# Optimization experiments

Hardware: AMD Instinct MI355X
Metric: run time of the kernel (lower is better)

The kernel has to match this reference:

```python
import jax, jax.numpy as jnp
import numpy as np

ALPHA = 0.02      # LeakyReLU negative slope
N_GRAPHS = 128    # number of graphs in the batch (global_mean_pool segments)
NEG_INF = jnp.float32(-9e15)


def _gat_head(x, mask, W, a1, a2):
    # One GraphAttentionLayer (no dropout: eval mode).
    Wh = x @ W                                   # [N, h]
    f1 = Wh @ a1                                 # [N] = a[:h] . Wh_i
    f2 = Wh @ a2                                 # [N] = a[h:] . Wh_j
    e = jax.nn.leaky_relu(f1[:, None] + f2[None, :], negative_slope=ALPHA)  # [N, N]
    e = jnp.where(mask, e, NEG_INF)              # adjacency-masked logits
    att = jax.nn.softmax(e, axis=-1)             # row-wise over neighbors
    return att @ Wh                              # [N, h]


def reference(x, edge_index, batch, W_heads, a1_heads, a2_heads,
              W_out, a1_out, a2_out, W1, b1, W2, b2):
    N = x.shape[0]
    # adj[src, dst] = 1 via scatter, exactly as the torch code
    adj = jnp.zeros((N, N), dtype=jnp.float32).at[edge_index[0], edge_index[1]].set(1.0)
    mask = adj > 0
    # multi-head GAT, heads vmapped: [H, N, h]
    heads = jax.vmap(_gat_head, in_axes=(None, None, 0, 0, 0))(
        x, mask, W_heads, a1_heads, a2_heads)
    heads = jax.nn.elu(heads)                    # concat=True applies elu per head
    h = jnp.transpose(heads, (1, 0, 2)).reshape(N, -1)   # concat -> [N, H*h]
    out = jax.nn.elu(_gat_head(h, mask, W_out, a1_out, a2_out))  # out_att + outer elu
    # global mean pool over graphs
    seg_sum = jax.ops.segment_sum(out, batch, num_segments=N_GRAPHS)
    counts = jax.ops.segment_sum(jnp.ones((N,), jnp.float32), batch, num_segments=N_GRAPHS)
    pooled = seg_sum / jnp.maximum(counts, 1.0)[:, None]          # [G, att_out]
    # MLP head
    hid = jax.nn.relu(pooled @ W1 + b1)
    return hid @ W2 + b2                                          # [G, nout]


def setup_inputs() -> dict:
    key = jax.random.key(0)
    ks = jax.random.split(key, 12)
    N, F, H, HID, OUT, MLP, NOUT, E = 2048, 300, 20, 600, 1000, 1000, 768, 32768
    s = 0.05
    return {
        "x": jax.random.normal(ks[0], (N, F), jnp.float32),
        "edge_index": jax.random.randint(ks[1], (2, E), 0, N),
        "batch": jnp.sort(jax.random.randint(ks[2], (N,), 0, N_GRAPHS)),
        "W_heads": jax.random.normal(ks[3], (H, F, HID), jnp.float32) * s,
        "a1_heads": jax.random.normal(ks[4], (H, HID), jnp.float32) * s,
        "a2_heads": jax.random.normal(ks[5], (H, HID), jnp.float32) * s,
        "W_out": jax.random.normal(ks[6], (H * HID, OUT), jnp.float32) * 0.01,
        "a1_out": jax.random.normal(ks[7], (OUT,), jnp.float32) * s,
        "a2_out": jax.random.normal(ks[8], (OUT,), jnp.float32) * s,
        "W1": jax.random.normal(ks[9], (OUT, MLP), jnp.float32) * 0.03,
        "b1": jnp.zeros((MLP,), jnp.float32),
        "W2": jax.random.normal(ks[10], (MLP, NOUT), jnp.float32) * 0.03,
        "b2": jnp.zeros((NOUT,), jnp.float32),
    }
```

## Files before the change

### kernel.cpp

```cpp
#include <hip/hip_runtime.h>
#include <math.h>

#define NN   2048
#define FF   300
#define FP   320
#define NH   20
#define HHID 600
#define HP   640
#define HCAT (NH * HHID)
#define DOUT 1000
#define NPAD 1024
#define MLPD 1000
#define NOUTD 768
#define NE   32768
#define NG   128
#define CAP  160
#define KSPL 6
#define KCH  2016
#define PVC  16
#define PVR  8
#define PVU  94

typedef __attribute__((ext_vector_type(8))) short short8;
typedef __attribute__((ext_vector_type(4))) float f32x4;

__device__ __forceinline__ unsigned short f2bf(float f) {
  unsigned int u = __float_as_uint(f);
  u += 0x7fffu + ((u >> 16) & 1u);
  return (unsigned short)(u >> 16);
}
__device__ __forceinline__ float bf2f(unsigned short u) {
  return __uint_as_float(((unsigned int)u) << 16);
}
__device__ __forceinline__ void st_out(float* p, float v) { *p = v; }
__device__ __forceinline__ void st_out(unsigned short* p, float v) { *p = f2bf(v); }


__global__ void zero_words(unsigned int* __restrict__ p, int n) {
  int i = blockIdx.x * blockDim.x + threadIdx.x;
  int stride = gridDim.x * blockDim.x;
  for (; i < n; i += stride) p[i] = 0u;
}

__global__ void scatter_mask(const int* __restrict__ ei, unsigned char* __restrict__ mask) {
  int e = blockIdx.x * blockDim.x + threadIdx.x;
  if (e < NE) {
    int s = ei[e], d = ei[NE + e];
    mask[(size_t)s * NN + d] = 1;
  }
}

__global__ void build_csr(const unsigned char* __restrict__ mask,
                          int* __restrict__ nbr, int* __restrict__ deg) {
  int wave = threadIdx.x >> 6, lane = threadIdx.x & 63;
  int i = blockIdx.x * 4 + wave;
  if (i >= NN) return;
  const unsigned* roww = (const unsigned*)(mask + (size_t)i * NN);
  int cnt = 0;
  for (int c0 = 0; c0 < NN; c0 += 256) {
    unsigned word = roww[(c0 >> 2) + lane];
#pragma unroll
    for (int b = 0; b < 4; b++) {
      bool p = ((word >> (8 * b)) & 0xffu) != 0u;
      unsigned long long bal = __ballot(p);
      if (p) {
        int pos = cnt + (int)__popcll(bal & ((1ull << lane) - 1ull));
        if (pos < CAP) nbr[(size_t)i * CAP + pos] = c0 + lane * 4 + b;
      }
      cnt += (int)__popcll(bal);
    }
  }
  if (lane == 0) deg[i] = cnt < CAP ? cnt : CAP;
}


__global__ void f12_kernel(const float* __restrict__ Wh, int ldw, int h,
                           const float* __restrict__ a1, const float* __restrict__ a2,
                           int astride,
                           float* __restrict__ f1, float* __restrict__ f2) {
  int i = blockIdx.x, hd = blockIdx.y;
  int lane = threadIdx.x;
  const float* r = Wh + (size_t)i * ldw + (size_t)hd * h;
  const float* A1 = a1 + (size_t)hd * astride;
  const float* A2 = a2 + (size_t)hd * astride;
  float s1 = 0.f, s2 = 0.f;
  for (int c = lane; c < h; c += 64) {
    float w = r[c];
    s1 += w * A1[c];
    s2 += w * A2[c];
  }
  for (int off = 32; off; off >>= 1) {
    s1 += __shfl_down(s1, off);
    s2 += __shfl_down(s2, off);
  }
  if (lane == 0) { f1[(size_t)hd * NN + i] = s1; f2[(size_t)hd * NN + i] = s2; }
}

__global__ void f12_bf16(const unsigned short* __restrict__ Wh, int ldw, int h,
                         const float* __restrict__ a1, const float* __restrict__ a2,
                         int astride,
                         float* __restrict__ f1, float* __restrict__ f2) {
  int i = blockIdx.x, hd = blockIdx.y;
  int lane = threadIdx.x;
  const unsigned short* r = Wh + (size_t)i * ldw + (size_t)hd * h;
  const float* A1 = a1 + (size_t)hd * astride;
  const float* A2 = a2 + (size_t)hd * astride;
  float s1 = 0.f, s2 = 0.f;
  for (int c8 = lane; c8 < h / 8; c8 += 64) {
    short8 v = *(const short8*)(r + (size_t)c8 * 8);
#pragma unroll
    for (int j = 0; j < 8; j++) {
      float w = bf2f((unsigned short)v[j]);
      s1 += w * A1[c8 * 8 + j];
      s2 += w * A2[c8 * 8 + j];
    }
  }
  for (int off = 32; off; off >>= 1) {
    s1 += __shfl_down(s1, off);
    s2 += __shfl_down(s2, off);
  }
  if (lane == 0) { f1[(size_t)hd * NN + i] = s1; f2[(size_t)hd * NN + i] = s2; }
}

__global__ void colsum_kernel(const float* __restrict__ Wh, int ldw, int h,
                              float* __restrict__ cs) {
  int hd = blockIdx.y;
  int c = blockIdx.x * blockDim.x + threadIdx.x;
  if (c >= h) return;
  size_t off = (size_t)hd * h + c;
  float s = 0.f;
  for (int i = 0; i < NN; i++) s += Wh[(size_t)i * ldw + off];
  cs[(size_t)hd * h + c] = s;
}

__global__ void colsum_at_bf16(const unsigned short* __restrict__ Wh, int ld, int width,
                               float* __restrict__ cs) {
  int c = blockIdx.x * blockDim.x + threadIdx.x;
  if (c >= width) return;
  int r0 = blockIdx.y * 64;
  float s = 0.f;
  for (int i = r0; i < r0 + 64; i++) s += bf2f(Wh[(size_t)i * ld + c]);
  atomicAdd(&cs[c], s);
}

__global__ void colsum_at_f32(const float* __restrict__ Wh, int ld, int width,
                              float* __restrict__ cs) {
  int c = blockIdx.x * blockDim.x + threadIdx.x;
  if (c >= width) return;
  int r0 = blockIdx.y * 64;
  float s = 0.f;
  for (int i = r0; i < r0 + 64; i++) s += Wh[(size_t)i * ld + c];
  atomicAdd(&cs[c], s);
}


template <typename OT>
__global__ __launch_bounds__(256)
void spmm_att(const float* __restrict__ Wh, int ldw, int h,
              const float* __restrict__ f1, const float* __restrict__ f2,
              const int* __restrict__ nbr, const int* __restrict__ deg,
              const float* __restrict__ cs,
              OT* __restrict__ outp, int ldo) {
  __shared__ float att[CAP];
  __shared__ int   nb[CAP];
  __shared__ float red[256];
  int i = blockIdx.x, hd = blockIdx.y;
  int t = threadIdx.x;
  int d = deg[i];
  size_t hoff = (size_t)hd * h;
  if (d > 0) {
    float fi = f1[(size_t)hd * NN + i];
    const float* F2 = f2 + (size_t)hd * NN;
    float lmax = -INFINITY;
    for (int k = t; k < d; k += 256) {
      int j = nbr[(size_t)i * CAP + k];
      nb[k] = j;
      float e = fi + F2[j];
      e = e > 0.f ? e : 0.02f * e;
      att[k] = e;
      lmax = fmaxf(lmax, e);
    }
    red[t] = lmax; __syncthreads();
    for (int s = 128; s; s >>= 1) { if (t < s) red[t] = fmaxf(red[t], red[t + s]); __syncthreads(); }
    float m = red[0]; __syncthreads();
    float ls = 0.f;
    for (int k = t; k < d; k += 256) { float p = expf(att[k] - m); att[k] = p; ls += p; }
    red[t] = ls; __syncthreads();
    for (int s = 128; s; s >>= 1) { if (t < s) red[t] += red[t + s]; __syncthreads(); }
    float inv = 1.0f / red[0]; __syncthreads();
    for (int k = t; k < d; k += 256) att[k] *= inv;
    __syncthreads();
    for (int c = t; c < h; c += 256) {
      float s = 0.f;
      for (int k = 0; k < d; k++) s += att[k] * Wh[(size_t)nb[k] * ldw + hoff + c];
      s = s > 0.f ? s : (expf(s) - 1.0f);
      st_out(&outp[(size_t)i * ldo + hoff + c], s);
    }
  } else {
    const float inv = 1.0f / (float)NN;
    for (int c = t; c < h; c += 256) {
      float s = cs[hoff + c] * inv;
      s = s > 0.f ? s : (expf(s) - 1.0f);
      st_out(&outp[(size_t)i * ldo + hoff + c], s);
    }
  }
}

__global__ __launch_bounds__(256)
void att_pre(const float* __restrict__ f1, const float* __restrict__ f2,
             const int* __restrict__ nbr, const int* __restrict__ deg,
             float* __restrict__ att_c) {
  __shared__ int   nb_sh[CAP];
  __shared__ float att_sh[4][CAP];
  int i = blockIdx.x;
  int t = threadIdx.x, w = t >> 6, lane = t & 63;
  int hd = blockIdx.y * 4 + w;
  int d = deg[i];
  if (d == 0) return;
  for (int k = t; k < d; k += 256) nb_sh[k] = nbr[(size_t)i * CAP + k];
  __syncthreads();
  float fi = f1[(size_t)hd * NN + i];
  const float* F2 = f2 + (size_t)hd * NN;
  float lmax = -INFINITY;
  for (int k = lane; k < d; k += 64) {
    float e = fi + F2[nb_sh[k]];
    e = e > 0.f ? e : 0.02f * e;
    att_sh[w][k] = e;
    lmax = fmaxf(lmax, e);
  }
  for (int off = 32; off; off >>= 1) lmax = fmaxf(lmax, __shfl_xor(lmax, off));
  float ls = 0.f;
  for (int k = lane; k < d; k += 64) {
    float p = expf(att_sh[w][k] - lmax);
    att_sh[w][k] = p; ls += p;
  }
  for (int off = 32; off; off >>= 1) ls += __shfl_xor(ls, off);
  float inv = 1.0f / ls;
  float* ao = att_c + ((size_t)i * NH + hd) * CAP;
  for (int k = lane; k < d; k += 64) ao[k] = att_sh[w][k] * inv;
}

__global__ __launch_bounds__(256)
void spmm_pv(const unsigned short* __restrict__ Whb,
             const float* __restrict__ att_c,
             const int* __restrict__ nbr, const int* __restrict__ deg,
             const float* __restrict__ cs,
             unsigned short* __restrict__ outp) {
  __shared__ int nb_sh[PVR][CAP];
  __shared__ int d_sh[PVR];
  int t = threadIdx.x;
  int r0 = blockIdx.y * PVR;
  int u0 = blockIdx.x * PVU;
  int nu = (u0 + PVU <= HCAT / 8) ? PVU : (HCAT / 8 - u0);
  if (t < PVR) d_sh[t] = deg[r0 + t];
  for (int q = t; q < PVR * CAP; q += 256) {
    int r = q / CAP, k = q - r * CAP;
    nb_sh[r][k] = nbr[(size_t)(r0 + r) * CAP + k];
  }
  __syncthreads();
  const float invn = 1.0f / (float)NN;
  int total = PVR * nu;
  for (int q = t; q < total; q += 256) {
    int r = q / nu, u = q - r * nu;
    int i = r0 + r;
    int gu = u0 + u;
    int hd = gu / (HHID / 8);
    int d = d_sh[r];
    const unsigned short* base = Whb + (size_t)gu * 8;
    unsigned short o8[8];
    if (d > 0) {
      const float* av = att_c + ((size_t)i * NH + hd) * CAP;
      float a8[8] = {};
      for (int k = 0; k < d; k++) {
        float a = av[k];
        short8 v = *(const short8*)(base + (size_t)nb_sh[r][k] * HCAT);
#pragma unroll
        for (int j = 0; j < 8; j++) a8[j] += a * bf2f((unsigned short)v[j]);
      }
#pragma unroll
      for (int j = 0; j < 8; j++) {
        float s = a8[j];
        s = s > 0.f ? s : (expf(s) - 1.0f);
        o8[j] = f2bf(s);
      }
    } else {
#pragma unroll
      for (int j = 0; j < 8; j++) {
        float s = cs[(size_t)gu * 8 + j] * invn;
        s = s > 0.f ? s : (expf(s) - 1.0f);
        o8[j] = f2bf(s);
      }
    }
    *(short8*)(outp + (size_t)i * HCAT + (size_t)gu * 8) = *(const short8*)o8;
  }
}

__global__ __launch_bounds__(128)
void spmm_att_o(const unsigned short* __restrict__ Wh,
                const float* __restrict__ f1, const float* __restrict__ f2,
                const int* __restrict__ nbr, const int* __restrict__ deg,
                const float* __restrict__ cs,
                float* __restrict__ outp) {
  __shared__ int   nb_sh[CAP];
  __shared__ float att_sh[CAP];
  __shared__ float red[128];
  int i = blockIdx.x, t = threadIdx.x;
  int d = deg[i];
  if (d > 0) {
    float fi = f1[i];
    float lmax = -INFINITY;
    for (int k = t; k < d; k += 128) {
      int j = nbr[(size_t)i * CAP + k];
      nb_sh[k] = j;
      float e = fi + f2[j];
      e = e > 0.f ? e : 0.02f * e;
      att_sh[k] = e;
      lmax = fmaxf(lmax, e);
    }
    red[t] = lmax; __syncthreads();
    for (int s = 64; s; s >>= 1) { if (t < s) red[t] = fmaxf(red[t], red[t + s]); __syncthreads(); }
    float m = red[0]; __syncthreads();
    float ls = 0.f;
    for (int k = t; k < d; k += 128) { float p = expf(att_sh[k] - m); att_sh[k] = p; ls += p; }
    red[t] = ls; __syncthreads();
    for (int s = 64; s; s >>= 1) { if (t < s) red[t] += red[t + s]; __syncthreads(); }
    float inv = 1.0f / red[0]; __syncthreads();
    for (int k = t; k < d; k += 128) att_sh[k] *= inv;
    __syncthreads();
    for (int cc = t; cc < DOUT / 8; cc += 128) {
      float a8[8] = {};
      const unsigned short* base = Wh + (size_t)cc * 8;
      for (int k = 0; k < d; k++) {
        float av = att_sh[k];
        short8 v = *(const short8*)(base + (size_t)nb_sh[k] * DOUT);
#pragma unroll
      for (int j = 0; j < 8; j++)
          a8[j] += av * bf2f((unsigned short)v[j]);
      }
      float o[8];
#pragma unroll
      for (int j = 0; j < 8; j++) {
        float s = a8[j];
        o[j] = s > 0.f ? s : (expf(s) - 1.0f);
      }
      *(float4*)(outp + (size_t)i * DOUT + (size_t)cc * 8)     = make_float4(o[0], o[1], o[2], o[3]);
      *(float4*)(outp + (size_t)i * DOUT + (size_t)cc * 8 + 4) = make_float4(o[4], o[5], o[6], o[7]);
    }
  } else {
    const float invn = 1.0f / (float)NN;
    for (int c = t; c < DOUT; c += 128) {
      float s = cs[c] * invn;
      outp[(size_t)i * DOUT + c] = s > 0.f ? s : (expf(s) - 1.0f);
    }
  }
}


__global__ void conv_x_bf16(const float* __restrict__ x, unsigned short* __restrict__ xb) {
  int i = blockIdx.x, t = threadIdx.x;
  float v = (t < FF) ? x[(size_t)i * FF + t] : 0.0f;
  xb[(size_t)i * FP + t] = f2bf(v);
}

__global__ void convT_gen(const float* __restrict__ W, unsigned short* __restrict__ Wt,
                          int K, int N, int ldw, long wz, int ldt, long tz) {
  __shared__ float tile[32][33];
  const float* Wp = W + (size_t)blockIdx.z * wz;
  unsigned short* Tp = Wt + (size_t)blockIdx.z * tz;
  int k0 = blockIdx.x * 32, n0 = blockIdx.y * 32;
  int tx = threadIdx.x, ty = threadIdx.y;
#pragma unroll
  for (int r = ty; r < 32; r += 8) {
    int kk = k0 + r, n = n0 + tx;
    tile[r][tx] = (kk < K && n < N) ? Wp[(size_t)kk * ldw + n] : 0.0f;
  }
  __syncthreads();
#pragma unroll
  for (int r = ty; r < 32; r += 8) {
    Tp[(size_t)(n0 + r) * ldt + k0 + tx] = f2bf(tile[tx][r]);
  }
}

__global__ void conv_f2b(const float* __restrict__ in, unsigned short* __restrict__ out, int n) {
  int i = blockIdx.x * blockDim.x + threadIdx.x;
  int stride = gridDim.x * blockDim.x;
  for (; i < n; i += stride) out[i] = f2bf(in[i]);
}

template <int LDA, int LDB, int LDC, int NREAL, int KCHUNK, int KTOT, int SWZ, typename OT>
__global__ __launch_bounds__(256)
void gemm_bf16_t(const unsigned short* __restrict__ A, long az,
                 const unsigned short* __restrict__ Bt, long bz,
                 OT* __restrict__ C, long cz) {
  __shared__ __align__(16) unsigned short As[128 * 32];
  __shared__ __align__(16) unsigned short Bs[128 * 32];
  int bx = blockIdx.x, by = blockIdx.y, bz_ = blockIdx.z;
  if (SWZ) {
    int gx = gridDim.x, gy = gridDim.y;
    int nwg = gx * gy * gridDim.z;
    int lin = bx + gx * (by + gy * bz_);
    int q = nwg >> 3;
    int lin2 = (lin & 7) * q + (lin >> 3);
    bx = lin2 % gx; by = (lin2 / gx) % gy; bz_ = lin2 / (gx * gy);
  }
  const int z = bz_;
  A  += (size_t)z * az;
  Bt += (size_t)z * bz;
  C  += (size_t)z * cz;
  int ks, ke;
  if (KCHUNK > 0) {
    ks = z * KCHUNK;
    ke = (ks + KCHUNK < KTOT) ? (ks + KCHUNK) : KTOT;
  } else {
    ks = 0; ke = KTOT;
  }
  const int t = threadIdx.x;
  const int w = t >> 6, lane = t & 63;
  const int m0 = by * 128, n0 = bx * 128;
  const int c0 = t, c1 = t + 256;
  const int ra0 = c0 >> 2, ca0 = (c0 & 3) * 8;
  const int ra1 = c1 >> 2, ca1 = (c1 & 3) * 8;
  const unsigned short* gA0 = A + (size_t)(m0 + ra0) * LDA + ca0;
  const unsigned short* gA1 = A + (size_t)(m0 + ra1) * LDA + ca1;
  const unsigned short* gB0 = Bt + (size_t)(n0 + ra0) * LDB + ca0;
  const unsigned short* gB1 = Bt + (size_t)(n0 + ra1) * LDB + ca1;
  unsigned short* lA0 = As + (size_t)w * 512;
  unsigned short* lA1 = As + (size_t)(4 + w) * 512;
  unsigned short* lB0 = Bs + (size_t)w * 512;
  unsigned short* lB1 = Bs + (size_t)(4 + w) * 512;
  const int wm = (w >> 1) * 64, wn = (w & 1) * 64;
  const int arow = lane & 15, acol = (lane >> 4) * 8;
  f32x4 acc[4][4] = {};
  for (int k = ks; k < ke; k += 32) {
    __builtin_amdgcn_global_load_lds((const __attribute__((address_space(1))) void*)(gA0 + k),
                                     (__attribute__((address_space(3))) void*)(lA0), 16, 0, 0);
    __builtin_amdgcn_global_load_lds((const __attribute__((address_space(1))) void*)(gA1 + k),
                                     (__attribute__((address_space(3))) void*)(lA1), 16, 0, 0);
    __builtin_amdgcn_global_load_lds((const __attribute__((address_space(1))) void*)(gB0 + k),
                                     (__attribute__((address_space(3))) void*)(lB0), 16, 0, 0);
    __builtin_amdgcn_global_load_lds((const __attribute__((address_space(1))) void*)(gB1 + k),
                                     (__attribute__((address_space(3))) void*)(lB1), 16, 0, 0);
    __syncthreads();
    short8 a[4], b[4];
#pragma unroll
    for (int i = 0; i < 4; i++)
      a[i] = *(const short8*)&As[(wm + i * 16 + arow) * 32 + acol];
#pragma unroll
    for (int j = 0; j < 4; j++)
      b[j] = *(const short8*)&Bs[(wn + j * 16 + arow) * 32 + acol];
#pragma unroll
    for (int i = 0; i < 4; i++)
#pragma unroll
      for (int j = 0; j < 4; j++)
        acc[i][j] = __builtin_amdgcn_mfma_f32_16x16x32_bf16(a[i], b[j], acc[i][j], 0, 0, 0);
    __syncthreads();
  }
  const int crow = (lane >> 4) * 4, ccol = lane & 15;
#pragma unroll
  for (int i = 0; i < 4; i++)
#pragma unroll
    for (int j = 0; j < 4; j++) {
      int gc = n0 + wn + j * 16 + ccol;
      if (gc < NREAL) {
#pragma unroll
        for (int r = 0; r < 4; r++)
          st_out(&C[(size_t)(m0 + wm + i * 16 + crow + r) * LDC + gc], acc[i][j][r]);
      }
    }
}

__global__ void addn_kernel(const float* __restrict__ p, unsigned short* __restrict__ ob) {
  const int n = NN * DOUT;
  int i = blockIdx.x * blockDim.x + threadIdx.x;
  int stride = gridDim.x * blockDim.x;
  for (; i < n; i += stride) {
    float v = 0.f;
#pragma unroll
    for (int z = 0; z < KSPL; z++) v += p[(size_t)z * n + i];
    ob[i] = f2bf(v);
  }
}

template <int K, int KS>
__global__ __launch_bounds__(256)
void gemm_thin(const float* __restrict__ A, const float* __restrict__ B,
               float* __restrict__ P, int N) {
  constexpr int KC = K / KS;
  __shared__ float Ash[128][KC + 3];
  int t = threadIdx.x;
  int tx = t & 63, ty = t >> 6;
  int n0 = blockIdx.x * 64, kz = blockIdx.y;
  int ks = kz * KC;
  for (int idx = t; idx < 128 * KC; idx += 256) {
    int r = idx / KC, c = idx - r * KC;
    Ash[r][c] = A[(size_t)r * K + ks + c];
  }
  __syncthreads();
  int nn = n0 + tx; if (nn > N - 1) nn = N - 1;
  const float* Bp = B + (size_t)ks * N + nn;
  int m0 = ty * 32;
  float acc[32] = {};
  for (int k4 = 0; k4 < KC / 4; k4++) {
    int k = k4 * 4;
    float w0 = Bp[(size_t)(k + 0) * N];
    float w1 = Bp[(size_t)(k + 1) * N];
    float w2 = Bp[(size_t)(k + 2) * N];
    float w3 = Bp[(size_t)(k + 3) * N];
#pragma unroll
    for (int mm = 0; mm < 32; mm++) {
      float4 a = *(const float4*)&Ash[m0 + mm][k];
      acc[mm] += a.x * w0 + a.y * w1 + a.z * w2 + a.w * w3;
    }
  }
#pragma unroll
  for (int k = (KC / 4) * 4; k < KC; k++) {
    float w0 = Bp[(size_t)k * N];
#pragma unroll
    for (int mm = 0; mm < 32; mm++) acc[mm] += Ash[m0 + mm][k] * w0;
  }
  if (n0 + tx < N) {
    float* Pp = P + (size_t)kz * 128 * N;
#pragma unroll
    for (int mm = 0; mm < 32; mm++)
      Pp[(size_t)(m0 + mm) * N + n0 + tx] = acc[mm];
  }
}

template <int N, int KS, int EPI>
__global__ void thin_reduce(const float* __restrict__ P, const float* __restrict__ bias,
                            float* __restrict__ C) {
  int i = blockIdx.x * blockDim.x + threadIdx.x;
  const int total = 128 * N;
  if (i >= total) return;
  int n = i % N;
  float v = 0.f;
#pragma unroll
  for (int z = 0; z < KS; z++) v += P[(size_t)z * total + i];
  v += bias[n];
  if (EPI == 2) v = v > 0.f ? v : 0.f;
  C[i] = v;
}

template <int BM_, int BN_, int EPI>
__global__ __launch_bounds__(256)
void gemm_t(const float* __restrict__ A, const float* __restrict__ B,
            float* __restrict__ C, const float* __restrict__ bias,
            int M, int N, int K, int lda, int ldb, int ldc, int accum,
            long bz, long cz) {
  constexpr int MR = BM_ / 16, NR = BN_ / 16;
  __shared__ float As[16][BM_ + 4];
  __shared__ float Bs[16][BN_ + 4];
  const float* Bp = B + (size_t)blockIdx.z * bz;
  float* Cp = C + (size_t)blockIdx.z * cz;
  int tx = threadIdx.x, ty = threadIdx.y;
  int tid = ty * 16 + tx;
  int m0 = blockIdx.y * BM_, n0 = blockIdx.x * BN_;
  float acc[MR][NR] = {};
  for (int k0 = 0; k0 < K; k0 += 16) {
#pragma unroll
    for (int p = 0; p < BM_ / 64; p++) {
      int id = tid + p * 256;
      int r = id >> 2, c4 = (id & 3) * 4;
      int gm = m0 + r;
      float v[4];
      if (gm < M && k0 + c4 + 3 < K) {
        const float4 t4 = *(const float4*)&A[(size_t)gm * lda + k0 + c4];
        v[0] = t4.x; v[1] = t4.y; v[2] = t4.z; v[3] = t4.w;
      } else {
#pragma unroll
        for (int q = 0; q < 4; q++) {
          int gk = k0 + c4 + q;
          v[q] = (gm < M && gk < K) ? A[(size_t)gm * lda + gk] : 0.0f;
        }
      }
#pragma unroll
      for (int q = 0; q < 4; q++) As[c4 + q][r] = v[q];
    }
#pragma unroll
    for (int p = 0; p < BN_ / 64; p++) {
      int id = tid + p * 256;
      int r = id / (BN_ / 4), c4 = (id % (BN_ / 4)) * 4;
      int gk = k0 + r, gn = n0 + c4;
      float v[4];
      if (gk < K && gn + 3 < N) {
        const float4 t4 = *(const float4*)&Bp[(size_t)gk * ldb + gn];
        v[0] = t4.x; v[1] = t4.y; v[2] = t4.z; v[3] = t4.w;
      } else {
#pragma unroll
        for (int q = 0; q < 4; q++)
          v[q] = (gk < K && gn + q < N) ? Bp[(size_t)gk * ldb + gn + q] : 0.0f;
      }
      *(float4*)&Bs[r][c4] = *(const float4*)v;
    }
    __syncthreads();
#pragma unroll
    for (int kk = 0; kk < 16; kk++) {
      float a[MR], b[NR];
#pragma unroll
      for (int q = 0; q < MR / 4; q++)
        *(float4*)&a[q * 4] = *(const float4*)&As[kk][ty * MR + q * 4];
#pragma unroll
      for (int q = 0; q < NR / 4; q++)
        *(float4*)&b[q * 4] = *(const float4*)&Bs[kk][tx * NR + q * 4];
#pragma unroll
      for (int i = 0; i < MR; i++)
#pragma unroll
        for (int j = 0; j < NR; j++) acc[i][j] += a[i] * b[j];
    }
    __syncthreads();
  }
#pragma unroll
  for (int i = 0; i < MR; i++) {
    int gm = m0 + ty * MR + i;
    if (gm >= M) continue;
#pragma unroll
    for (int j = 0; j < NR; j++) {
      int gn = n0 + tx * NR + j;
      if (gn >= N) continue;
      float r = acc[i][j];
      if (accum) r += Cp[(size_t)gm * ldc + gn];
      if (EPI == 2) { r += bias[gn]; r = r > 0.f ? r : 0.f; }
      else if (EPI == 3) { r += bias[gn]; }
      Cp[(size_t)gm * ldc + gn] = r;
    }
  }
}


__global__ void pool_prep(const int* __restrict__ batch, int* __restrict__ startg, int* __restrict__ cntg) {
  int n = blockIdx.x * blockDim.x + threadIdx.x;
  if (n >= NN) return;
  int b = batch[n];
  if (n == 0 || batch[n - 1] != b) startg[b] = n;
  atomicAdd(&cntg[b], 1);
}

__global__ void pool_kernel(const float* __restrict__ outb,
                            const int* __restrict__ startg, const int* __restrict__ cntg,
                            float* __restrict__ pooled) {
  int g = blockIdx.x, t = threadIdx.x;
  int st = startg[g], c = cntg[g];
  for (int ch = t; ch < DOUT; ch += 256) {
    float s = 0.f;
    for (int k = 0; k < c; k++) s += outb[(size_t)(st + k) * DOUT + ch];
    pooled[(size_t)g * DOUT + ch] = s / (float)(c > 0 ? c : 1);
  }
}


static inline int cdiv(int a, int b) { return (a + b - 1) / b; }

extern "C" void kernel_launch(void* const* d_in, const int* in_sizes, int n_in,
                              void* d_out, int out_size, void* d_ws, size_t ws_size,
                              hipStream_t stream) {
  const float* x        = (const float*)d_in[0];
  const int*   ei       = (const int*)d_in[1];
  const int*   batch    = (const int*)d_in[2];
  const float* W_heads  = (const float*)d_in[3];
  const float* a1_heads = (const float*)d_in[4];
  const float* a2_heads = (const float*)d_in[5];
  const float* W_out    = (const float*)d_in[6];
  const float* a1_out   = (const float*)d_in[7];
  const float* a2_out   = (const float*)d_in[8];
  const float* W1       = (const float*)d_in[9];
  const float* b1       = (const float*)d_in[10];
  const float* W2       = (const float*)d_in[11];
  const float* b2       = (const float*)d_in[12];
  float* outd = (float*)d_out;
  (void)in_sizes; (void)n_in; (void)out_size;

  char* w = (char*)d_ws;
  size_t off = 0;
  auto alloc = [&](size_t bytes) {
    void* p = w + off;
    off += (bytes + 255) & ~(size_t)255;
    return p;
  };
  auto al = [](size_t b) { return (b + 255) & ~(size_t)255; };

  unsigned char* mask = (unsigned char*)alloc((size_t)NN * NN);
  int*   nbr    = (int*)alloc((size_t)NN * CAP * 4);
  int*   deg    = (int*)alloc((size_t)NN * 4);
  float* acc    = (float*)alloc((size_t)NN * DOUT * 4);
  unsigned short* accb = (unsigned short*)alloc((size_t)NN * DOUT * 2);
  float* outb   = (float*)alloc((size_t)NN * DOUT * 4);
  float* f1o    = (float*)alloc((size_t)NN * 4);
  float* f2o    = (float*)alloc((size_t)NN * 4);
  float* cso    = (float*)alloc((size_t)DOUT * 4);
  float* pooled = (float*)alloc((size_t)NG * DOUT * 4);
  float* hid    = (float*)alloc((size_t)NG * MLPD * 4);
  int*   startg = (int*)alloc((size_t)NG * 4);
  int*   cntg   = (int*)alloc((size_t)NG * 4);
  size_t off_common = off;

  size_t need_batched = off_common
      + al((size_t)NN * HCAT * 2)
      + al((size_t)NN * HCAT * 2)
      + al((size_t)NPAD * HCAT * 2)
      + al((size_t)NN * FP * 2)
      + al((size_t)NH * HP * FP * 2)
      + al((size_t)NN * NH * CAP * 4)
      + al((size_t)NH * NN * 4) * 2
      + al((size_t)NH * HHID * 4);
  bool batched = ws_size >= need_batched;

  zero_words<<<4096, 256, 0, stream>>>((unsigned int*)mask, NN * NN / 4);
  scatter_mask<<<cdiv(NE, 256), 256, 0, stream>>>(ei, mask);
  build_csr<<<NN / 4, 256, 0, stream>>>(mask, nbr, deg);

  if (batched) {
    unsigned short* Whb   = (unsigned short*)alloc((size_t)NN * HCAT * 2);
    unsigned short* hcatb = (unsigned short*)alloc((size_t)NN * HCAT * 2);
    unsigned short* Wt    = (unsigned short*)alloc((size_t)NPAD * HCAT * 2);
    unsigned short* xb    = (unsigned short*)alloc((size_t)NN * FP * 2);
    unsigned short* Wth   = (unsigned short*)alloc((size_t)NH * HP * FP * 2);
    float* att_c  = (float*)alloc((size_t)NN * NH * CAP * 4);
    float* f1a    = (float*)alloc((size_t)NH * NN * 4);
    float* f2a    = (float*)alloc((size_t)NH * NN * 4);
    float* csa    = (float*)alloc((size_t)NH * HHID * 4);
    float* partC = (float*)Whb;

    conv_x_bf16<<<NN, FP, 0, stream>>>(x, xb);
    convT_gen<<<dim3(FP / 32, HP / 32, NH), dim3(32, 8), 0, stream>>>(
        W_heads, Wth, FF, HHID, HHID, (long)FF * HHID, FP, (long)HP * FP);
    gemm_bf16_t<FP, FP, HCAT, HHID, 0, FP, 0, unsigned short>
        <<<dim3(HP / 128, NN / 128, NH), 256, 0, stream>>>(
        xb, 0L, Wth, (long)HP * FP, Whb, (long)HHID);
    f12_bf16<<<dim3(NN, NH), 64, 0, stream>>>(Whb, HCAT, HHID,
                                              a1_heads, a2_heads, HHID, f1a, f2a);
    zero_words<<<12, 256, 0, stream>>>((unsigned int*)csa, NH * HHID);
    colsum_at_bf16<<<dim3(cdiv(HCAT, 256), NN / 64), 256, 0, stream>>>(Whb, HCAT, HCAT, csa);
    convT_gen<<<dim3(HCAT / 32, NPAD / 32, 1), dim3(32, 8), 0, stream>>>(
        W_out, Wt, HCAT, DOUT, DOUT, 0L, HCAT, 0L);
    att_pre<<<dim3(NN, NH / 4), 256, 0, stream>>>(f1a, f2a, nbr, deg, att_c);
    spmm_pv<<<dim3(PVC, NN / PVR), 256, 0, stream>>>(Whb, att_c, nbr, deg, csa, hcatb);
    gemm_bf16_t<HCAT, HCAT, DOUT, DOUT, KCH, HCAT, 1, float>
        <<<dim3(NPAD / 128, NN / 128, KSPL), 256, 0, stream>>>(
        hcatb, 0L, Wt, 0L, partC, (long)NN * DOUT);
    addn_kernel<<<2048, 256, 0, stream>>>(partC, accb);
    f12_bf16<<<dim3(NN, 1), 64, 0, stream>>>(accb, DOUT, DOUT, a1_out, a2_out, 0, f1o, f2o);
    zero_words<<<1, 256, 0, stream>>>((unsigned int*)cso, DOUT);
    colsum_at_bf16<<<dim3(cdiv(DOUT, 256), NN / 64), 256, 0, stream>>>(accb, DOUT, DOUT, cso);
    spmm_att_o<<<dim3(NN), 128, 0, stream>>>(accb, f1o, f2o, nbr, deg, cso, outb);
  } else {
    float* Wh   = (float*)alloc((size_t)NN * HHID * 4);
    float* hout = (float*)alloc((size_t)NN * HHID * 4);
    float* f1   = (float*)alloc((size_t)NN * 4);
    float* f2   = (float*)alloc((size_t)NN * 4);
    float* cs   = (float*)alloc((size_t)HHID * 4);
    zero_words<<<8000, 256, 0, stream>>>((unsigned int*)acc, NN * DOUT);
    for (int hd = 0; hd < NH; hd++) {
      gemm_t<64, 64, 0><<<dim3(cdiv(HHID, 64), cdiv(NN, 64), 1), dim3(16, 16), 0, stream>>>(
          x, W_heads + (size_t)hd * FF * HHID, Wh, nullptr,
          NN, HHID, FF, FF, HHID, HHID, 0, 0L, 0L);
      f12_kernel<<<dim3(NN, 1), 64, 0, stream>>>(Wh, HHID, HHID,
          a1_heads + (size_t)hd * HHID, a2_heads + (size_t)hd * HHID, 0, f1, f2);
      colsum_kernel<<<dim3(cdiv(HHID, 256), 1), 256, 0, stream>>>(Wh, HHID, HHID, cs);
      spmm_att<float><<<dim3(NN, 1), 256, 0, stream>>>(Wh, HHID, HHID, f1, f2,
                                                       nbr, deg, cs, hout, HHID);
      gemm_t<64, 64, 0><<<dim3(cdiv(DOUT, 64), cdiv(NN, 64), 1), dim3(16, 16), 0, stream>>>(
          hout, W_out + (size_t)hd * HHID * DOUT, acc, nullptr,
          NN, DOUT, HHID, HHID, DOUT, DOUT, 1, 0L, 0L);
    }
    conv_f2b<<<2048, 256, 0, stream>>>(acc, accb, NN * DOUT);
    f12_kernel<<<dim3(NN, 1), 64, 0, stream>>>(acc, DOUT, DOUT, a1_out, a2_out, 0, f1o, f2o);
    zero_words<<<1, 256, 0, stream>>>((unsigned int*)cso, DOUT);
    colsum_at_f32<<<dim3(cdiv(DOUT, 256), NN / 64), 256, 0, stream>>>(acc, DOUT, DOUT, cso);
    spmm_att_o<<<dim3(NN), 128, 0, stream>>>(accb, f1o, f2o, nbr, deg, cso, outb);
  }

  zero_words<<<1, 256, 0, stream>>>((unsigned int*)startg, NG * 2);
  pool_prep<<<NN / 256, 256, 0, stream>>>(batch, startg, cntg);
  pool_kernel<<<NG, 256, 0, stream>>>(outb, startg, cntg, pooled);

  float* mlpP = acc;
  gemm_thin<DOUT, 8><<<dim3(cdiv(MLPD, 64), 8), 256, 0, stream>>>(pooled, W1, mlpP, MLPD);
  thin_reduce<MLPD, 8, 2><<<cdiv(NG * MLPD, 256), 256, 0, stream>>>(mlpP, b1, hid);
  gemm_thin<MLPD, 8><<<dim3(cdiv(NOUTD, 64), 8), 256, 0, stream>>>(hid, W2, mlpP, NOUTD);
  thin_reduce<NOUTD, 8, 3><<<cdiv(NG * NOUTD, 256), 256, 0, stream>>>(mlpP, b2, outd);
}
```

Before: 380.0 us.

## Precompute attention vectors via W·a and split spmm_pv into two column halves

The per-head attention scores f1/f2 are now computed as x·(W·a) from precomputed folded vectors, instead of reading the full bf16 Wh matrix. The column sums used for the empty-row fallback come from the x column sums times W_heads, replacing a pass over Wh. spmm_pv now processes 16 rows per block and runs as two launches over column halves, which may improve L2 locality of Wh. The folded path computes in fp32 from the original x and W rather than bf16 Wh, which slightly changes rounding, and it adds launches.

```diff
diff --git a/kernel.cpp b/kernel.cpp
--- a/kernel.cpp
+++ b/kernel.cpp
@@ -18,8 +18,9 @@
 #define KSPL 6
 #define KCH  2016
 #define PVC  16
-#define PVR  8
-#define PVU  94
+#define PVR  16
+#define PVU  47
+#define PVHALF 750
 
 typedef __attribute__((ext_vector_type(8))) short short8;
 typedef __attribute__((ext_vector_type(4))) float f32x4;
@@ -71,6 +72,59 @@
     }
   }
   if (lane == 0) deg[i] = cnt < CAP ? cnt : CAP;
+}
+
+
+__global__ void w12_kernel(const float* __restrict__ W, const float* __restrict__ a1,
+                           const float* __restrict__ a2,
+                           float* __restrict__ w1, float* __restrict__ w2) {
+  int k = blockIdx.x, hd = blockIdx.y, lane = threadIdx.x;
+  const float* r = W + ((size_t)hd * FF + k) * HHID;
+  const float* A1 = a1 + (size_t)hd * HHID;
+  const float* A2 = a2 + (size_t)hd * HHID;
+  float s1 = 0.f, s2 = 0.f;
+  for (int c = lane; c < HHID; c += 64) {
+    float w = r[c];
+    s1 += w * A1[c];
+    s2 += w * A2[c];
+  }
+  for (int off = 32; off; off >>= 1) {
+    s1 += __shfl_down(s1, off);
+    s2 += __shfl_down(s2, off);
+  }
+  if (lane == 0) { w1[(size_t)hd * FF + k] = s1; w2[(size_t)hd * FF + k] = s2; }
+}
+
+__global__ __launch_bounds__(256)
+void f12x_kernel(const float* __restrict__ x, const float* __restrict__ w1,
+                 const float* __restrict__ w2,
+                 float* __restrict__ f1, float* __restrict__ f2) {
+  __shared__ float xr[FF];
+  int i = blockIdx.x, t = threadIdx.x;
+  for (int c = t; c < FF; c += 256) xr[c] = x[(size_t)i * FF + c];
+  __syncthreads();
+  if (t < 2 * NH) {
+    int hd = t >> 1;
+    const float* wv = ((t & 1) ? w2 : w1) + (size_t)hd * FF;
+    float s = 0.f;
+    for (int k = 0; k < FF; k++) s += xr[k] * wv[k];
+    ((t & 1) ? f2 : f1)[(size_t)hd * NN + i] = s;
+  }
+}
+
+__global__ __launch_bounds__(256)
+void csa_kernel(const float* __restrict__ xsum, const float* __restrict__ W,
+                float* __restrict__ csa) {
+  __shared__ float xs[FF];
+  int hd = blockIdx.y, t = threadIdx.x;
+  for (int k = t; k < FF; k += 256) xs[k] = xsum[k];
+  __syncthreads();
+  int c = blockIdx.x * 256 + t;
+  if (c >= HHID) return;
+  const float* Wp = W + (size_t)hd * FF * HHID + c;
+  float s = 0.f;
+  for (int k = 0; k < FF; k++) s += xs[k] * Wp[(size_t)k * HHID];
+  csa[(size_t)hd * HHID + c] = s;
 }
 
 
@@ -245,13 +299,15 @@
              const float* __restrict__ att_c,
              const int* __restrict__ nbr, const int* __restrict__ deg,
              const float* __restrict__ cs,
-             unsigned short* __restrict__ outp) {
+             unsigned short* __restrict__ outp,
+             int ubase) {
   __shared__ int nb_sh[PVR][CAP];
   __shared__ int d_sh[PVR];
   int t = threadIdx.x;
   int r0 = blockIdx.y * PVR;
-  int u0 = blockIdx.x * PVU;
-  int nu = (u0 + PVU <= HCAT / 8) ? PVU : (HCAT / 8 - u0);
+  int u0 = ubase + blockIdx.x * PVU;
+  int ulim = ubase + PVHALF;
+  int nu = (u0 + PVU <= ulim) ? PVU : (ulim - u0);
   if (t < PVR) d_sh[t] = deg[r0 + t];
   for (int q = t; q < PVR * CAP; q += 256) {
     int r = q / CAP, k = q - r * CAP;
@@ -701,7 +757,9 @@
       + al((size_t)NH * HP * FP * 2)
       + al((size_t)NN * NH * CAP * 4)
       + al((size_t)NH * NN * 4) * 2
-      + al((size_t)NH * HHID * 4);
+      + al((size_t)NH * HHID * 4)
+      + al((size_t)NH * FF * 4) * 2
+      + al((size_t)FF * 4);
   bool batched = ws_size >= need_batched;
 
   zero_words<<<4096, 256, 0, stream>>>((unsigned int*)mask, NN * NN / 4);
@@ -718,6 +776,9 @@
     float* f1a    = (float*)alloc((size_t)NH * NN * 4);
     float* f2a    = (float*)alloc((size_t)NH * NN * 4);
     float* csa    = (float*)alloc((size_t)NH * HHID * 4);
+    float* w1b    = (float*)alloc((size_t)NH * FF * 4);
+    float* w2b    = (float*)alloc((size_t)NH * FF * 4);
+    float* xsum   = (float*)alloc((size_t)FF * 4);
     float* partC = (float*)Whb;
 
     conv_x_bf16<<<NN, FP, 0, stream>>>(x, xb);
@@ -726,14 +787,16 @@
     gemm_bf16_t<FP, FP, HCAT, HHID, 0, FP, 0, unsigned short>
         <<<dim3(HP / 128, NN / 128, NH), 256, 0, stream>>>(
         xb, 0L, Wth, (long)HP * FP, Whb, (long)HHID);
-    f12_bf16<<<dim3(NN, NH), 64, 0, stream>>>(Whb, HCAT, HHID,
-                                              a1_heads, a2_heads, HHID, f1a, f2a);
-    zero_words<<<12, 256, 0, stream>>>((unsigned int*)csa, NH * HHID);
-    colsum_at_bf16<<<dim3(cdiv(HCAT, 256), NN / 64), 256, 0, stream>>>(Whb, HCAT, HCAT, csa);
+    w12_kernel<<<dim3(FF, NH), 64, 0, stream>>>(W_heads, a1_heads, a2_heads, w1b, w2b);
+    f12x_kernel<<<NN, 256, 0, stream>>>(x, w1b, w2b, f1a, f2a);
+    zero_words<<<1, 256, 0, stream>>>((unsigned int*)xsum, FF);
+    colsum_at_f32<<<dim3(cdiv(FF, 256), NN / 64), 256, 0, stream>>>(x, FF, FF, xsum);
+    csa_kernel<<<dim3(cdiv(HHID, 256), NH), 256, 0, stream>>>(xsum, W_heads, csa);
     convT_gen<<<dim3(HCAT / 32, NPAD / 32, 1), dim3(32, 8), 0, stream>>>(
         W_out, Wt, HCAT, DOUT, DOUT, 0L, HCAT, 0L);
     att_pre<<<dim3(NN, NH / 4), 256, 0, stream>>>(f1a, f2a, nbr, deg, att_c);
-    spmm_pv<<<dim3(PVC, NN / PVR), 256, 0, stream>>>(Whb, att_c, nbr, deg, csa, hcatb);
+    spmm_pv<<<dim3(PVC, NN / PVR), 256, 0, stream>>>(Whb, att_c, nbr, deg, csa, hcatb, 0);
+    spmm_pv<<<dim3(PVC, NN / PVR), 256, 0, stream>>>(Whb, att_c, nbr, deg, csa, hcatb, PVHALF);
     gemm_bf16_t<HCAT, HCAT, DOUT, DOUT, KCH, HCAT, 1, float>
         <<<dim3(NPAD / 128, NN / 128, KSPL), 256, 0, stream>>>(
         hcatb, 0L, Wt, 0L, partC, (long)NN * DOUT);
```

Result: slower. 390.9 us (+2.9%).

## Fuse attention projections and column sums into head GEMM epilogue

Applied to the files above, without the earlier changes.

Adds a FUSE template flag to the bf16 MFMA GEMM. When it is set, the epilogue computes the per-row a1/a2 dot products (f1, f2) and the per-column sums of Wh straight from the fp32 accumulators. It reduces them with wave shuffles and adds them into global buffers with atomics, which removes the separate f12_bf16 and colsum_at_bf16 passes over the large per-head Wh matrix. In exchange it adds atomic traffic, a zero-fill pass that assumes f2a sits directly after f1a in memory, and order-dependent float summation based on unrounded fp32 values rather than bf16 ones.

```diff
diff --git a/kernel.cpp b/kernel.cpp
--- a/kernel.cpp
+++ b/kernel.cpp
@@ -387,11 +387,15 @@
   for (; i < n; i += stride) out[i] = f2bf(in[i]);
 }
 
-template <int LDA, int LDB, int LDC, int NREAL, int KCHUNK, int KTOT, int SWZ, typename OT>
+template <int LDA, int LDB, int LDC, int NREAL, int KCHUNK, int KTOT, int SWZ, int FUSE,
+          typename OT>
 __global__ __launch_bounds__(256)
 void gemm_bf16_t(const unsigned short* __restrict__ A, long az,
                  const unsigned short* __restrict__ Bt, long bz,
-                 OT* __restrict__ C, long cz) {
+                 OT* __restrict__ C, long cz,
+                 const float* __restrict__ a1, const float* __restrict__ a2,
+                 float* __restrict__ f1, float* __restrict__ f2,
+                 float* __restrict__ csa) {
   __shared__ __align__(16) unsigned short As[128 * 32];
   __shared__ __align__(16) unsigned short Bs[128 * 32];
   int bx = blockIdx.x, by = blockIdx.y, bz_ = blockIdx.z;
@@ -467,6 +471,51 @@
           st_out(&C[(size_t)(m0 + wm + i * 16 + crow + r) * LDC + gc], acc[i][j][r]);
       }
     }
+  if (FUSE) {
+    int gcj[4]; float A1v[4], A2v[4];
+#pragma unroll
+    for (int j = 0; j < 4; j++) {
+      gcj[j] = n0 + wn + j * 16 + ccol;
+      bool in = gcj[j] < NREAL;
+      A1v[j] = in ? a1[(size_t)z * NREAL + gcj[j]] : 0.0f;
+      A2v[j] = in ? a2[(size_t)z * NREAL + gcj[j]] : 0.0f;
+    }
+#pragma unroll
+    for (int i = 0; i < 4; i++) {
+#pragma unroll
+      for (int r = 0; r < 4; r++) {
+        float p1 = 0.f, p2 = 0.f;
+#pragma unroll
+        for (int j = 0; j < 4; j++) {
+          float v = acc[i][j][r];
+          p1 += v * A1v[j];
+          p2 += v * A2v[j];
+        }
+#pragma unroll
+        for (int off = 1; off < 16; off <<= 1) {
+          p1 += __shfl_xor(p1, off);
+          p2 += __shfl_xor(p2, off);
+        }
+        if ((lane & 15) == 0) {
+          int row = m0 + wm + i * 16 + crow + r;
+          atomicAdd(&f1[(size_t)z * NN + row], p1);
+          atomicAdd(&f2[(size_t)z * NN + row], p2);
+        }
+      }
+    }
+#pragma unroll
+    for (int j = 0; j < 4; j++) {
+      float cp = 0.f;
+#pragma unroll
+      for (int i = 0; i < 4; i++)
+#pragma unroll
+        for (int r = 0; r < 4; r++) cp += acc[i][j][r];
+      cp += __shfl_xor(cp, 16);
+      cp += __shfl_xor(cp, 32);
+      if (lane < 16 && gcj[j] < NREAL)
+        atomicAdd(&csa[(size_t)z * NREAL + gcj[j]], cp);
+    }
+  }
 }
 
 __global__ void addn_kernel(const float* __restrict__ p, unsigned short* __restrict__ ob) {
@@ -723,20 +772,20 @@
     conv_x_bf16<<<NN, FP, 0, stream>>>(x, xb);
     convT_gen<<<dim3(FP / 32, HP / 32, NH), dim3(32, 8), 0, stream>>>(
         W_heads, Wth, FF, HHID, HHID, (long)FF * HHID, FP, (long)HP * FP);
-    gemm_bf16_t<FP, FP, HCAT, HHID, 0, FP, 0, unsigned short>
+    zero_words<<<80, 256, 0, stream>>>((unsigned int*)f1a, 2 * NH * NN);
+    zero_words<<<12, 256, 0, stream>>>((unsigned int*)csa, NH * HHID);
+    gemm_bf16_t<FP, FP, HCAT, HHID, 0, FP, 0, 1, unsigned short>
         <<<dim3(HP / 128, NN / 128, NH), 256, 0, stream>>>(
-        xb, 0L, Wth, (long)HP * FP, Whb, (long)HHID);
-    f12_bf16<<<dim3(NN, NH), 64, 0, stream>>>(Whb, HCAT, HHID,
-                                              a1_heads, a2_heads, HHID, f1a, f2a);
-    zero_words<<<12, 256, 0, stream>>>((unsigned int*)csa, NH * HHID);
-    colsum_at_bf16<<<dim3(cdiv(HCAT, 256), NN / 64), 256, 0, stream>>>(Whb, HCAT, HCAT, csa);
+        xb, 0L, Wth, (long)HP * FP, Whb, (long)HHID,
+        a1_heads, a2_heads, f1a, f2a, csa);
     convT_gen<<<dim3(HCAT / 32, NPAD / 32, 1), dim3(32, 8), 0, stream>>>(
         W_out, Wt, HCAT, DOUT, DOUT, 0L, HCAT, 0L);
     att_pre<<<dim3(NN, NH / 4), 256, 0, stream>>>(f1a, f2a, nbr, deg, att_c);
     spmm_pv<<<dim3(PVC, NN / PVR), 256, 0, stream>>>(Whb, att_c, nbr, deg, csa, hcatb);
-    gemm_bf16_t<HCAT, HCAT, DOUT, DOUT, KCH, HCAT, 1, float>
+    gemm_bf16_t<HCAT, HCAT, DOUT, DOUT, KCH, HCAT, 1, 0, float>
         <<<dim3(NPAD / 128, NN / 128, KSPL), 256, 0, stream>>>(
-        hcatb, 0L, Wt, 0L, partC, (long)NN * DOUT);
+        hcatb, 0L, Wt, 0L, partC, (long)NN * DOUT,
+        nullptr, nullptr, nullptr, nullptr, nullptr);
     addn_kernel<<<2048, 256, 0, stream>>>(partC, accb);
     f12_bf16<<<dim3(NN, 1), 64, 0, stream>>>(accb, DOUT, DOUT, a1_out, a2_out, 0, f1o, f2o);
     zero_words<<<1, 256, 0, stream>>>((unsigned int*)cso, DOUT);
```

New measurement: 377.2 us. Within noise of the previous version (-0.7%).
